# Kernel optimization log

Hardware: AMD Instinct MI355X
Metric: run time of the kernel (lower is better)

## Reference

```python
import jax, jax.numpy as jnp
import numpy as np

B, C, L = 16, 64, 512
L_P = 16
D_MODEL = 1024
STRIDE = 8
N_P = (L - L_P) // STRIDE + 2  # 64 patches
PERIOD = L // 2                # statsmodels period = series_input_length / 2


def setup_inputs() -> dict:
    key = jax.random.key(0)
    ks = jax.random.split(key, 11)
    s = 0.02  # small init scale for weights
    return {
        "data_x": jax.random.normal(ks[0], (B, C, L), jnp.float32),
        "gamma": jax.random.uniform(ks[1], (B, C, L), jnp.float32),
        "beta": jax.random.uniform(ks[2], (B, C, L), jnp.float32),
        "w_trend": jax.random.normal(ks[3], (L_P, L), jnp.float32) * s,
        "b_trend": jax.random.normal(ks[4], (L_P,), jnp.float32) * s,
        "w_seasonal": jax.random.normal(ks[5], (L_P, L), jnp.float32) * s,
        "b_seasonal": jax.random.normal(ks[6], (L_P,), jnp.float32) * s,
        "w_resid": jax.random.normal(ks[7], (L_P, L), jnp.float32) * s,
        "b_resid": jax.random.normal(ks[8], (L_P,), jnp.float32) * s,
        "w_g": jax.random.normal(ks[9], (D_MODEL, 3 * L_P), jnp.float32) * s,
        "b_g": jax.random.normal(ks[10], (D_MODEL,), jnp.float32) * s,
    }


def _decompose(x):
    """Vectorized statsmodels seasonal_decompose(model='additive', period=L//2).

    trend: centered moving average with filter [0.5,1,...,1,0.5]/p (even period),
           NaN edges -> replaced by 0 (as in the torch module).
    seasonal: per-phase nanmean of detrended, demeaned, tiled to length L.
    resid: detrended - seasonal on the valid (non-NaN) region, 0 elsewhere.
    x: [B, C, L] -> (trend, seasonal, resid) each [B, C, L].
    """
    p = PERIOD
    filt = jnp.concatenate([jnp.full((1,), 0.5, x.dtype),
                            jnp.ones((p - 1,), x.dtype),
                            jnp.full((1,), 0.5, x.dtype)]) / p  # len p+1 (p even)
    head = p // 2               # leading NaN count (filter is symmetric)
    nvalid = L - p              # valid trend samples
    xf = x.reshape(B * C, 1, L)
    tv = jax.lax.conv_general_dilated(xf, filt.reshape(1, 1, p + 1),
                                      (1,), "VALID")[:, 0, :]  # [BC, L-p]
    trend = jnp.zeros((B * C, L), x.dtype).at[:, head:head + nvalid].set(tv)
    dv = x.reshape(B * C, L)[:, head:head + nvalid] - tv  # detrended, valid region
    # per-phase nanmean over valid detrended samples
    phase = (head + jnp.arange(nvalid)) % p               # phase of each valid index
    sums = jnp.zeros((B * C, p), x.dtype).at[:, phase].add(dv)
    counts = jnp.zeros((p,), x.dtype).at[phase].add(1.0)
    pa = sums / counts                                    # period averages [BC, p]
    pa = pa - jnp.mean(pa, axis=1, keepdims=True)
    seasonal = jnp.tile(pa, (1, L // p))                  # L = 2p exactly
    resid = jnp.zeros((B * C, L), x.dtype).at[:, head:head + nvalid].set(
        dv - seasonal[:, head:head + nvalid])
    return (trend.reshape(B, C, L), seasonal.reshape(B, C, L),
            resid.reshape(B, C, L))


def reference(data_x, gamma, beta, w_trend, b_trend, w_seasonal, b_seasonal,
              w_resid, b_resid, w_g, b_g):
    # 'transformed': per-channel stats (dim=1), torch var is unbiased (ddof=1), epsi=0
    mean = jnp.mean(data_x, axis=1)
    var = jnp.var(data_x, axis=1, ddof=1)
    mean = (mean / jnp.sqrt(var))[:, None, :]             # [B,1,L] broadcast over C
    x = gamma * (data_x - mean) + beta
    x = jax.lax.stop_gradient(x)                          # season() detaches
    trend, seasonal, resid = _decompose(x)
    t = trend @ w_trend.T + b_trend                       # [B,C,L_p]
    s = seasonal @ w_seasonal.T + b_seasonal
    r = resid @ w_resid.T + b_resid
    feats = jnp.concatenate([t, s, r], axis=-1)           # [B,C,3*L_p]
    feats = jnp.broadcast_to(feats[:, :, None, :], (B, C, N_P, 3 * L_P))
    return feats @ w_g.T + b_g                            # [B,C,N_p,D_MODEL]
```

## Files before the change

### kernel.cpp

```cpp
#include <hip/hip_runtime.h>
#include <math.h>

#define BB   16
#define CC   64
#define LL   512
#define LP   16
#define DM   1024
#define NP   64
#define PRD  256
#define HEAD 128
#define NV   256

typedef float f32x4 __attribute__((ext_vector_type(4)));

__global__ __launch_bounds__(256) void fused_kernel(
    const float* __restrict__ dx,    const float* __restrict__ gamma,
    const float* __restrict__ beta,  const float* __restrict__ w_t,
    const float* __restrict__ b_t,   const float* __restrict__ w_s,
    const float* __restrict__ b_s,   const float* __restrict__ w_r,
    const float* __restrict__ b_r,   const float* __restrict__ w_g,
    const float* __restrict__ b_g,   float* __restrict__ out)
{
    __shared__ __align__(16) float xs[LL];
    __shared__ __align__(16) float pps[LL/2 + 1];
    __shared__ __align__(16) float tvs[NV];
    __shared__ __align__(16) float pas[PRD];
    __shared__ __align__(16) float feats[48];
    __shared__ __align__(16) float sres[DM];
    __shared__ float wsum[4];
    __shared__ float wred[4];

    const int tid  = threadIdx.x;
    const int lane = tid & 63;
    const int wv   = tid >> 6;
    const int bc   = blockIdx.x;
    const int b    = bc >> 6;
    const int cown = bc & 63;

    const float2* dxb = (const float2*)(dx + (size_t)b * CC * LL);
    float2 sv = make_float2(0.f, 0.f), qv = make_float2(0.f, 0.f);
    float2 xv = make_float2(0.f, 0.f);
#pragma unroll 8
    for (int c = 0; c < CC; ++c) {
        float2 v = dxb[c * 256 + tid];
        if (c == cown) xv = v;
        sv.x += v.x;       sv.y += v.y;
        qv.x += v.x * v.x; qv.y += v.y * v.y;
    }
    float2 mp;
    {
        float mx = sv.x * (1.0f / CC), my = sv.y * (1.0f / CC);
        float vx = (qv.x - (float)CC * mx * mx) * (1.0f / (CC - 1));
        float vy = (qv.y - (float)CC * my * my) * (1.0f / (CC - 1));
        mp.x = mx / sqrtf(vx);
        mp.y = my / sqrtf(vy);
    }

    const size_t base = (size_t)bc * LL;
    float2 gv = ((const float2*)(gamma + base))[tid];
    float2 bv = ((const float2*)(beta  + base))[tid];
    float2 xp;
    xp.x = gv.x * (xv.x - mp.x) + bv.x;
    xp.y = gv.y * (xv.y - mp.y) + bv.y;
    ((float2*)xs)[tid] = xp;

    float v = xp.x + xp.y;
#pragma unroll
    for (int d = 1; d < 64; d <<= 1) {
        float t = __shfl_up(v, d, 64);
        if (lane >= d) v += t;
    }
    if (lane == 63) wsum[wv] = v;
    __syncthreads();
    float off = 0.f;
    for (int w = 0; w < wv; ++w) off += wsum[w];
    pps[tid + 1] = v + off;
    if (tid == 0) pps[0] = 0.f;
    __syncthreads();

    const int i  = tid;
    const int k2 = i + 257;
    const float Pi = pps[i  >> 1] + ((i  & 1) ? xs[i  & ~1] : 0.f);
    const float Pk = pps[k2 >> 1] + ((k2 & 1) ? xs[k2 & ~1] : 0.f);
    const float tv = (Pk - Pi - 0.5f * (xs[i] + xs[i + 256])) * (1.0f / 256.0f);
    tvs[i] = tv;
    const float dv = xs[HEAD + i] - tv;

    float r = dv;
#pragma unroll
    for (int m = 32; m; m >>= 1) r += __shfl_xor(r, m, 64);
    if (lane == 0) wred[wv] = r;
    __syncthreads();
    const float mdv = (wred[0] + wred[1] + wred[2] + wred[3]) * (1.0f / 256.0f);

    pas[(i + 128) & 255] = dv - mdv;
    __syncthreads();

    {
        const int g  = tid >> 4;
        const int ln = tid & 15;
        const f32x4* wt4  = (const f32x4*)(w_t + g * LL + HEAD);
        const f32x4* ws4a = (const f32x4*)(w_s + g * LL);
        const f32x4* ws4b = (const f32x4*)(w_s + g * LL + PRD);
        const f32x4* wr4  = (const f32x4*)(w_r + g * LL + HEAD);
        const f32x4* tv4  = (const f32x4*)tvs;
        const f32x4* pa4  = (const f32x4*)pas;
        float at = 0.f, as = 0.f, ar = 0.f;
#pragma unroll
        for (int q = 0; q < 4; ++q) {
            const int m = ln * 4 + q;
            f32x4 t  = tv4[m],  p  = pa4[m];
            f32x4 a  = wt4[m];
            f32x4 s1 = ws4a[m], s2 = ws4b[m];
            f32x4 rr = wr4[m];
            at += t.x * a.x + t.y * a.y + t.z * a.z + t.w * a.w;
            as += p.x * (s1.x + s2.x) + p.y * (s1.y + s2.y)
                + p.z * (s1.z + s2.z) + p.w * (s1.w + s2.w);
            ar += rr.x + rr.y + rr.z + rr.w;
        }
#pragma unroll
        for (int msk = 8; msk; msk >>= 1) {
            at += __shfl_xor(at, msk, 64);
            as += __shfl_xor(as, msk, 64);
            ar += __shfl_xor(ar, msk, 64);
        }
        if (ln == 0) {
            feats[g]      = at + b_t[g];
            feats[16 + g] = as + b_s[g];
            feats[32 + g] = mdv * ar + b_r[g];
        }
    }
    __syncthreads();

    {
        const int qsl = lane & 3;
        float fs[12];
#pragma unroll
        for (int k = 0; k < 12; ++k) fs[k] = feats[qsl * 12 + k];

        const f32x4* wg4 = (const f32x4*)w_g;
#pragma unroll 4
        for (int p = 0; p < 16; ++p) {
            const int drow = p * 64 + wv * 16 + (lane >> 2);
            const int wbase = (p * 64 + wv * 16) * 12 + 3 * lane;
            f32x4 w0 = wg4[wbase + 0];
            f32x4 w1 = wg4[wbase + 1];
            f32x4 w2 = wg4[wbase + 2];
            float acc = fs[0]*w0.x + fs[1]*w0.y + fs[2]*w0.z + fs[3]*w0.w
                      + fs[4]*w1.x + fs[5]*w1.y + fs[6]*w1.z + fs[7]*w1.w
                      + fs[8]*w2.x + fs[9]*w2.y + fs[10]*w2.z + fs[11]*w2.w;
            acc += __shfl_xor(acc, 1, 64);
            acc += __shfl_xor(acc, 2, 64);
            if (qsl == 0) sres[drow] = acc + b_g[drow];
        }
    }
    __syncthreads();

    const f32x4* s4 = (const f32x4*)sres;
    const f32x4 v0 = s4[lane];
    const f32x4 v1 = s4[64 + lane];
    const f32x4 v2 = s4[128 + lane];
    const f32x4 v3 = s4[192 + lane];
    f32x4* op = (f32x4*)out + (size_t)bc * (NP * DM / 4)
              + (size_t)(wv * 16) * (DM / 4) + lane;
#pragma unroll
    for (int n = 0; n < 16; ++n) {
        op[n * (DM / 4) +   0] = v0;
        op[n * (DM / 4) +  64] = v1;
        op[n * (DM / 4) + 128] = v2;
        op[n * (DM / 4) + 192] = v3;
    }
}

extern "C" void kernel_launch(void* const* d_in, const int* in_sizes, int n_in,
                              void* d_out, int out_size, void* d_ws, size_t ws_size,
                              hipStream_t stream) {
    const float* dx    = (const float*)d_in[0];
    const float* gamma = (const float*)d_in[1];
    const float* beta  = (const float*)d_in[2];
    const float* w_t   = (const float*)d_in[3];
    const float* b_t   = (const float*)d_in[4];
    const float* w_s   = (const float*)d_in[5];
    const float* b_s   = (const float*)d_in[6];
    const float* w_r   = (const float*)d_in[7];
    const float* b_r   = (const float*)d_in[8];
    const float* w_g   = (const float*)d_in[9];
    const float* b_g   = (const float*)d_in[10];
    float* out = (float*)d_out;

    fused_kernel<<<BB * CC, 256, 0, stream>>>(
        dx, gamma, beta, w_t, b_t, w_s, b_s, w_r, b_r, w_g, b_g, out);
}
```

Before: 65.26 us.

## Split compute and broadcast store into two kernels over workspace buffer

The fused kernel now writes only its 1024-float result row per (b,c) to a workspace buffer. A second kernel with one block per output patch row (65536 blocks) reads that row and writes it out. This spreads the 256 MB broadcast write across far more blocks to raise store parallelism, at the cost of an extra launch and a round trip through the workspace.

Result: slower. 73.88 us (+13.2%).

```diff
diff --git a/kernel.cpp b/kernel.cpp
--- a/kernel.cpp
+++ b/kernel.cpp
@@ -13,13 +13,13 @@
 
 typedef float f32x4 __attribute__((ext_vector_type(4)));
 
-__global__ __launch_bounds__(256) void fused_kernel(
+__global__ __launch_bounds__(256) void compute_kernel(
     const float* __restrict__ dx,    const float* __restrict__ gamma,
     const float* __restrict__ beta,  const float* __restrict__ w_t,
     const float* __restrict__ b_t,   const float* __restrict__ w_s,
     const float* __restrict__ b_s,   const float* __restrict__ w_r,
     const float* __restrict__ b_r,   const float* __restrict__ w_g,
-    const float* __restrict__ b_g,   float* __restrict__ out)
+    const float* __restrict__ b_g,   float* __restrict__ resbuf)
 {
     __shared__ __align__(16) float xs[LL];
     __shared__ __align__(16) float pps[LL/2 + 1];
@@ -156,20 +156,17 @@
     }
     __syncthreads();
 
-    const f32x4* s4 = (const f32x4*)sres;
-    const f32x4 v0 = s4[lane];
-    const f32x4 v1 = s4[64 + lane];
-    const f32x4 v2 = s4[128 + lane];
-    const f32x4 v3 = s4[192 + lane];
-    f32x4* op = (f32x4*)out + (size_t)bc * (NP * DM / 4)
-              + (size_t)(wv * 16) * (DM / 4) + lane;
-#pragma unroll
-    for (int n = 0; n < 16; ++n) {
-        op[n * (DM / 4) +   0] = v0;
-        op[n * (DM / 4) +  64] = v1;
-        op[n * (DM / 4) + 128] = v2;
-        op[n * (DM / 4) + 192] = v3;
-    }
+    ((f32x4*)resbuf)[(size_t)bc * 256 + tid] = ((const f32x4*)sres)[tid];
+}
+
+__global__ __launch_bounds__(256) void store_kernel(
+    const float* __restrict__ resbuf, float* __restrict__ out)
+{
+    const int tid = threadIdx.x;
+    const int k   = blockIdx.x;
+    const int bc  = k >> 6;
+    const f32x4 v = ((const f32x4*)resbuf)[(size_t)bc * 256 + tid];
+    ((f32x4*)out)[(size_t)k * 256 + tid] = v;
 }
 
 extern "C" void kernel_launch(void* const* d_in, const int* in_sizes, int n_in,
@@ -187,7 +184,9 @@
     const float* w_g   = (const float*)d_in[9];
     const float* b_g   = (const float*)d_in[10];
     float* out = (float*)d_out;
+    float* resbuf = (float*)d_ws;
 
-    fused_kernel<<<BB * CC, 256, 0, stream>>>(
-        dx, gamma, beta, w_t, b_t, w_s, b_s, w_r, b_r, w_g, b_g, out);
+    compute_kernel<<<BB * CC, 256, 0, stream>>>(
+        dx, gamma, beta, w_t, b_t, w_s, b_s, w_r, b_r, w_g, b_g, resbuf);
+    store_kernel<<<BB * CC * NP, 256, 0, stream>>>(resbuf, out);
 }
```
